# Optimization experiments

Measured on AMD Instinct MI355X. Metric: run time of the kernel, lower is better.

Reference implementation:

```python
import jax, jax.numpy as jnp
import numpy as np

H_LAT = 64   # latent height (original_shape H)
W_LAT = 64   # latent width  (original_shape W)
COND_LEN = 77  # text tokens per regional condition


def _resize_nearest_exact(m, H, W):
    # matches torch F.interpolate(mode='nearest-exact') for a 2D mask
    h0, w0 = m.shape
    ih = jnp.floor((jnp.arange(H) + 0.5) * (h0 / H)).astype(jnp.int32)
    iw = jnp.floor((jnp.arange(W) + 0.5) * (w0 / W)).astype(jnp.int32)
    return m[ih][:, iw]


def setup_inputs() -> dict:
    key = jax.random.key(0)
    kq, kk, kv, km = jax.random.split(key, 4)
    b, qlen, inner = 2, H_LAT * W_LAT, 512
    klen = 4 * COND_LEN  # 4 regions x 77 tokens
    q = jax.random.normal(kq, (b, qlen, inner), dtype=jnp.float32)
    k = jax.random.normal(kk, (b, klen, inner), dtype=jnp.float32)
    v = jax.random.normal(kv, (b, klen, inner), dtype=jnp.float32)
    dd_masks = jax.random.uniform(km, (4, 32, 32), dtype=jnp.float32)
    # ensure full spatial coverage (region 0 = global) so no softmax row is all-masked
    dd_masks = dd_masks.at[0].set(1.0)
    return {"q": q, "k": k, "v": v, "dd_masks": dd_masks, "heads": 8}


def reference(q, k, v, dd_masks, heads):
    b, qlen, inner = q.shape
    dh = inner // heads
    # [b, heads, seq, dh]
    qh = q.reshape(b, qlen, heads, dh).transpose(0, 2, 1, 3)
    kh = k.reshape(b, -1, heads, dh).transpose(0, 2, 1, 3)
    vh = v.reshape(b, -1, heads, dh).transpose(0, 2, 1, 3)

    # build DenseDiffusion mask: each region mask resized to HxW, flattened,
    # and repeated over that region's COND_LEN key columns
    R = dd_masks.shape[0]
    resized = jax.vmap(lambda m: _resize_nearest_exact(m, H_LAT, W_LAT))(dd_masks)  # [R,H,W]
    flat = resized.reshape(R, H_LAT * W_LAT).T            # [HW, R]
    masks = jnp.repeat(flat, COND_LEN, axis=1)            # [HW, R*COND_LEN]
    mask_bool = masks > 0.5                               # [HW, klen]
    mask_scale = (H_LAT * W_LAT) / jnp.sum(masks, axis=0, keepdims=True)  # [1, klen]

    scale = 1.0 / np.sqrt(dh).astype(np.float32)
    attn = jnp.einsum('bhqd,bhkd->bhqk', qh, kh) * scale  # [b,h,HW,klen]
    attn = attn * mask_scale                              # broadcast over b,h,q
    attn = jnp.where(mask_bool, attn, -jnp.inf)
    w = jax.nn.softmax(attn, axis=-1)
    out = jnp.einsum('bhqk,bhkd->bhqd', w, vh)
    return out.transpose(0, 2, 1, 3).reshape(b, qlen, heads * dh)
```

## Files before the change

kernel.cpp:

```cpp
#include <hip/hip_runtime.h>
#include <hip/hip_bf16.h>

typedef __attribute__((ext_vector_type(8))) short short8;
typedef __attribute__((ext_vector_type(4))) float floatx4;

#define HW_TOK 4096
#define KLEN 308
#define DH 64
#define INNER 512

#define VBASE (KLEN * 64)
#define LDS_TOTAL (VBASE + DH * 320)

__device__ __forceinline__ unsigned short f2bf(float f) {
    union { float f; unsigned u; } x; x.f = f;
    unsigned u = x.u;
    return (unsigned short)((u + 0x7FFFu + ((u >> 16) & 1u)) >> 16);
}
__device__ __forceinline__ unsigned pk2bf(float a, float b) {
    return ((unsigned)f2bf(b) << 16) | (unsigned)f2bf(a);
}

__global__ __launch_bounds__(512, 2)
void dd_attn_kernel(const float* __restrict__ q,
                    const float* __restrict__ k,
                    const float* __restrict__ v,
                    const float* __restrict__ dd,
                    float* __restrict__ out) {
    __shared__ unsigned short KV[LDS_TOTAL];

    const int tid  = threadIdx.x;
    const int lane = tid & 63;
    const int wave = tid >> 6;
    const int quad = lane >> 4;
    const int l15  = lane & 15;
    const int kxor = l15 & 7;

    const int bid = blockIdx.x;
    const int bh  = bid >> 5;
    const int grp = bid & 31;
    const int b = bh >> 3, h = bh & 7;

    const float* qp = q + (size_t)b * HW_TOK * INNER + h * DH;
    const float* kp = k + (size_t)b * KLEN * INNER + h * DH;
    const float* vp = v + (size_t)b * KLEN * INNER + h * DH;
    float* op = out + (size_t)b * HW_TOK * INNER + h * DH;

    for (int e = tid; e < KLEN * 32; e += 512) {
        int row = e >> 5, d2 = e & 31;
        float2 f = *(const float2*)(kp + (size_t)row * INNER + 2 * d2);
        int c = d2 >> 2;
        int off = row * 64 + (((c ^ (row & 7)) << 3) | ((d2 & 3) << 1));
        *(unsigned*)&KV[off] = pk2bf(f.x, f.y);
    }
    for (int e = tid; e < KLEN * 32; e += 512) {
        int col = e >> 5, d2 = e & 31;
        float2 f = *(const float2*)(vp + (size_t)col * INNER + 2 * d2);
        int c = col >> 3, c7 = col & 7;
        int r0 = 2 * d2, r1 = r0 + 1;
        KV[VBASE + r0 * 320 + (((c & ~7) | ((c ^ r0) & 7)) << 3) + c7] = f2bf(f.x);
        KV[VBASE + r1 * 320 + (((c & ~7) | ((c ^ r1) & 7)) << 3) + c7] = f2bf(f.y);
    }
    for (int e = tid; e < DH * 12; e += 512) {
        int row = e / 12, col = 308 + e % 12;
        int c = col >> 3, c7 = col & 7;
        KV[VBASE + row * 320 + (((c & ~7) | ((c ^ row) & 7)) << 3) + c7] = 0;
    }

    float rsum = 0.f;
    {
        const float* dp = dd + quad * 1024 + l15 * 4;
        #pragma unroll
        for (int j = 0; j < 16; ++j) {
            float4 f = *(const float4*)(dp + j * 64);
            rsum += f.x + f.y + f.z + f.w;
        }
        #pragma unroll
        for (int off = 1; off < 16; off <<= 1) rsum += __shfl_xor(rsum, off);
    }
    float rsc[4];
    #pragma unroll
    for (int r = 0; r < 4; ++r)
        rsc[r] = 4096.0f / (4.0f * __shfl(rsum, r * 16 + l15));

    __syncthreads();

    const int q0 = (grp * 8 + wave) * 16;
    const int qrow = q0 + l15;

    const float* qr = qp + (size_t)qrow * INNER + quad * 8;
    float4 f0 = *(const float4*)(qr);
    float4 f1 = *(const float4*)(qr + 4);
    float4 f2 = *(const float4*)(qr + 32);
    float4 f3 = *(const float4*)(qr + 36);
    short8 qa0, qa1;
    qa0[0]=(short)f2bf(f0.x); qa0[1]=(short)f2bf(f0.y); qa0[2]=(short)f2bf(f0.z); qa0[3]=(short)f2bf(f0.w);
    qa0[4]=(short)f2bf(f1.x); qa0[5]=(short)f2bf(f1.y); qa0[6]=(short)f2bf(f1.z); qa0[7]=(short)f2bf(f1.w);
    qa1[0]=(short)f2bf(f2.x); qa1[1]=(short)f2bf(f2.y); qa1[2]=(short)f2bf(f2.z); qa1[3]=(short)f2bf(f2.w);
    qa1[4]=(short)f2bf(f3.x); qa1[5]=(short)f2bf(f3.y); qa1[6]=(short)f2bf(f3.z); qa1[7]=(short)f2bf(f3.w);

    const int mi = (qrow >> 7) * 32 + ((qrow & 63) >> 1);
    float coef[4];
    #pragma unroll
    for (int r = 0; r < 4; ++r)
        coef[r] = (dd[r * 1024 + mi] > 0.5f) ? 0.125f * rsc[r] : -1.0f;

    float m_run = -INFINITY, l_run = 0.f;
    floatx4 oacc[4] = {{0,0,0,0},{0,0,0,0},{0,0,0,0},{0,0,0,0}};

    #pragma unroll
    for (int ch = 0; ch < 2; ++ch) {
        floatx4 acc[10];
        #pragma unroll
        for (int t = 0; t < 10; ++t) {
            int row = (ch * 10 + t) * 16 + l15;
            short8 ka0 = *(const short8*)&KV[row * 64 + ((quad       ^ kxor) << 3)];
            short8 ka1 = *(const short8*)&KV[row * 64 + (((4 + quad) ^ kxor) << 3)];
            floatx4 c = {0.f, 0.f, 0.f, 0.f};
            c = __builtin_amdgcn_mfma_f32_16x16x32_bf16(ka0, qa0, c, 0, 0, 0);
            c = __builtin_amdgcn_mfma_f32_16x16x32_bf16(ka1, qa1, c, 0, 0, 0);
            acc[t] = c;
        }

        float mloc = -INFINITY;
        #pragma unroll
        for (int t = 0; t < 10; ++t) {
            #pragma unroll
            for (int r = 0; r < 4; ++r) {
                int kc = (ch * 10 + t) * 16 + quad * 4 + r;
                float cf = (kc < 77) ? coef[0] : (kc < 154) ? coef[1]
                         : (kc < 231) ? coef[2] : (kc < 308) ? coef[3] : -1.0f;
                float sv = (cf > 0.f) ? acc[t][r] * cf : -INFINITY;
                acc[t][r] = sv;
                mloc = fmaxf(mloc, sv);
            }
        }
        mloc = fmaxf(mloc, __shfl_xor(mloc, 16));
        mloc = fmaxf(mloc, __shfl_xor(mloc, 32));

        float m_new = fmaxf(m_run, mloc);
        float alpha = __expf(m_run - m_new);
        float lloc = 0.f;
        #pragma unroll
        for (int t = 0; t < 10; ++t) {
            #pragma unroll
            for (int r = 0; r < 4; ++r) {
                float p = __expf(acc[t][r] - m_new);
                acc[t][r] = p;
                lloc += p;
            }
        }
        lloc += __shfl_xor(lloc, 16);
        lloc += __shfl_xor(lloc, 32);
        l_run = l_run * alpha + lloc;
        m_run = m_new;
        #pragma unroll
        for (int n = 0; n < 4; ++n)
            #pragma unroll
            for (int r = 0; r < 4; ++r) oacc[n][r] *= alpha;

        const int sl0 = ((quad & 1) << 5) + l15;
        const int sl1 = sl0 + 16;
        const bool hi = (quad >= 2);
        #pragma unroll
        for (int c32 = 0; c32 < 5; ++c32) {
            floatx4 pA = acc[2 * c32];
            floatx4 pB = acc[2 * c32 + 1];
            unsigned uA0 = pk2bf(pA[0], pA[1]), uA1 = pk2bf(pA[2], pA[3]);
            unsigned uB0 = pk2bf(pB[0], pB[1]), uB1 = pk2bf(pB[2], pB[3]);
            unsigned xA0 = (unsigned)__shfl((int)uA0, sl0), xB0 = (unsigned)__shfl((int)uB0, sl0);
            unsigned xA1 = (unsigned)__shfl((int)uA1, sl0), xB1 = (unsigned)__shfl((int)uB1, sl0);
            unsigned yA0 = (unsigned)__shfl((int)uA0, sl1), yB0 = (unsigned)__shfl((int)uB0, sl1);
            unsigned yA1 = (unsigned)__shfl((int)uA1, sl1), yB1 = (unsigned)__shfl((int)uB1, sl1);
            union { short8 s; unsigned u[4]; } pu;
            pu.u[0] = hi ? xB0 : xA0;
            pu.u[1] = hi ? xB1 : xA1;
            pu.u[2] = hi ? yB0 : yA0;
            pu.u[3] = hi ? yB1 : yA1;
            #pragma unroll
            for (int n = 0; n < 4; ++n) {
                int row = n * 16 + l15;
                int c = ch * 20 + c32 * 4 + quad;
                int cs = (c & ~7) | ((c ^ kxor) & 7);
                short8 va = *(const short8*)&KV[VBASE + row * 320 + (cs << 3)];
                oacc[n] = __builtin_amdgcn_mfma_f32_16x16x32_bf16(va, pu.s, oacc[n], 0, 0, 0);
            }
        }
    }

    const float inv = 1.0f / l_run;
    #pragma unroll
    for (int n = 0; n < 4; ++n) {
        float4 o;
        o.x = oacc[n][0] * inv;
        o.y = oacc[n][1] * inv;
        o.z = oacc[n][2] * inv;
        o.w = oacc[n][3] * inv;
        *(float4*)&op[(size_t)qrow * INNER + n * 16 + quad * 4] = o;
    }
}

extern "C" void kernel_launch(void* const* d_in, const int* in_sizes, int n_in,
                              void* d_out, int out_size, void* d_ws, size_t ws_size,
                              hipStream_t stream) {
    const float* q  = (const float*)d_in[0];
    const float* k  = (const float*)d_in[1];
    const float* v  = (const float*)d_in[2];
    const float* dd = (const float*)d_in[3];
    float* out = (float*)d_out;
    dd_attn_kernel<<<dim3(512), dim3(512), 0, stream>>>(q, k, v, dd, out);
}
```

Baseline: 105.1 us.

## Process two query tiles per wave to reuse K/V fragments, halve grid

Each wave now handles 32 query rows as two 16-row tiles. Every K and V fragment read from LDS feeds MFMAs for both tiles, and the grid shrinks to 256 blocks, so K/V staging into LDS is repeated half as often. The probability tile now reaches the PV MFMA operand layout through a per-wave LDS buffer instead of cross-lane shuffles. The V transpose staging is rewritten as coalesced per-lane column loads with 16-byte LDS stores. The trade-off is higher register pressure (launch bounds drop to one block per CU) and fewer blocks to hide latency.

```diff
diff --git a/kernel.cpp b/kernel.cpp
--- a/kernel.cpp
+++ b/kernel.cpp
@@ -9,8 +9,11 @@
 #define DH 64
 #define INNER 512
 
-#define VBASE (KLEN * 64)
-#define LDS_TOTAL (VBASE + DH * 320)
+#define KROWS 320
+#define VSTRU 328
+#define VBASE (KROWS * 64)
+#define KV_TOTAL (VBASE + DH * VSTRU)
+#define PSTR 40
 
 __device__ __forceinline__ unsigned short f2bf(float f) {
     union { float f; unsigned u; } x; x.f = f;
@@ -21,24 +24,24 @@
     return ((unsigned)f2bf(b) << 16) | (unsigned)f2bf(a);
 }
 
-__global__ __launch_bounds__(512, 2)
+__global__ __launch_bounds__(512, 1)
 void dd_attn_kernel(const float* __restrict__ q,
                     const float* __restrict__ k,
                     const float* __restrict__ v,
                     const float* __restrict__ dd,
                     float* __restrict__ out) {
-    __shared__ unsigned short KV[LDS_TOTAL];
+    __shared__ unsigned short KV[KV_TOTAL];
+    __shared__ unsigned short Pb[8][2][16][PSTR];
 
     const int tid  = threadIdx.x;
     const int lane = tid & 63;
     const int wave = tid >> 6;
     const int quad = lane >> 4;
     const int l15  = lane & 15;
-    const int kxor = l15 & 7;
 
     const int bid = blockIdx.x;
-    const int bh  = bid >> 5;
-    const int grp = bid & 31;
+    const int bh  = bid >> 4;
+    const int grp = bid & 15;
     const int b = bh >> 3, h = bh & 7;
 
     const float* qp = q + (size_t)b * HW_TOK * INNER + h * DH;
@@ -53,20 +56,21 @@
         int off = row * 64 + (((c ^ (row & 7)) << 3) | ((d2 & 3) << 1));
         *(unsigned*)&KV[off] = pk2bf(f.x, f.y);
     }
-    for (int e = tid; e < KLEN * 32; e += 512) {
-        int col = e >> 5, d2 = e & 31;
-        float2 f = *(const float2*)(vp + (size_t)col * INNER + 2 * d2);
-        int c = col >> 3, c7 = col & 7;
-        int r0 = 2 * d2, r1 = r0 + 1;
-        KV[VBASE + r0 * 320 + (((c & ~7) | ((c ^ r0) & 7)) << 3) + c7] = f2bf(f.x);
-        KV[VBASE + r1 * 320 + (((c & ~7) | ((c ^ r1) & 7)) << 3) + c7] = f2bf(f.y);
-    }
-    for (int e = tid; e < DH * 12; e += 512) {
-        int row = e / 12, col = 308 + e % 12;
-        int c = col >> 3, c7 = col & 7;
-        KV[VBASE + row * 320 + (((c & ~7) | ((c ^ row) & 7)) << 3) + c7] = 0;
-    }
-
+    #pragma unroll
+    for (int i = 0; i < 5; ++i) {
+        int cq = wave + 8 * i;
+        float f[8];
+        #pragma unroll
+        for (int j = 0; j < 8; ++j) {
+            int col = cq * 8 + j;
+            f[j] = (col < KLEN) ? vp[(size_t)col * INNER + lane] : 0.f;
+        }
+        union { short8 s; unsigned u[4]; } vv;
+        #pragma unroll
+        for (int j = 0; j < 4; ++j) vv.u[j] = pk2bf(f[2 * j], f[2 * j + 1]);
+        int swz = (cq & ~7) | ((cq ^ (lane & 7)) & 7);
+        *(short8*)&KV[VBASE + lane * VSTRU + (swz << 3)] = vv.s;
+    }
     float rsum = 0.f;
     {
         const float* dp = dd + quad * 1024 + l15 * 4;
@@ -85,118 +89,138 @@
 
     __syncthreads();
 
-    const int q0 = (grp * 8 + wave) * 16;
-    const int qrow = q0 + l15;
-
-    const float* qr = qp + (size_t)qrow * INNER + quad * 8;
-    float4 f0 = *(const float4*)(qr);
-    float4 f1 = *(const float4*)(qr + 4);
-    float4 f2 = *(const float4*)(qr + 32);
-    float4 f3 = *(const float4*)(qr + 36);
-    short8 qa0, qa1;
-    qa0[0]=(short)f2bf(f0.x); qa0[1]=(short)f2bf(f0.y); qa0[2]=(short)f2bf(f0.z); qa0[3]=(short)f2bf(f0.w);
-    qa0[4]=(short)f2bf(f1.x); qa0[5]=(short)f2bf(f1.y); qa0[6]=(short)f2bf(f1.z); qa0[7]=(short)f2bf(f1.w);
-    qa1[0]=(short)f2bf(f2.x); qa1[1]=(short)f2bf(f2.y); qa1[2]=(short)f2bf(f2.z); qa1[3]=(short)f2bf(f2.w);
-    qa1[4]=(short)f2bf(f3.x); qa1[5]=(short)f2bf(f3.y); qa1[6]=(short)f2bf(f3.z); qa1[7]=(short)f2bf(f3.w);
-
-    const int mi = (qrow >> 7) * 32 + ((qrow & 63) >> 1);
-    float coef[4];
-    #pragma unroll
-    for (int r = 0; r < 4; ++r)
-        coef[r] = (dd[r * 1024 + mi] > 0.5f) ? 0.125f * rsc[r] : -1.0f;
-
-    float m_run = -INFINITY, l_run = 0.f;
-    floatx4 oacc[4] = {{0,0,0,0},{0,0,0,0},{0,0,0,0},{0,0,0,0}};
-
-    #pragma unroll
-    for (int ch = 0; ch < 2; ++ch) {
-        floatx4 acc[10];
-        #pragma unroll
-        for (int t = 0; t < 10; ++t) {
-            int row = (ch * 10 + t) * 16 + l15;
-            short8 ka0 = *(const short8*)&KV[row * 64 + ((quad       ^ kxor) << 3)];
-            short8 ka1 = *(const short8*)&KV[row * 64 + (((4 + quad) ^ kxor) << 3)];
-            floatx4 c = {0.f, 0.f, 0.f, 0.f};
-            c = __builtin_amdgcn_mfma_f32_16x16x32_bf16(ka0, qa0, c, 0, 0, 0);
-            c = __builtin_amdgcn_mfma_f32_16x16x32_bf16(ka1, qa1, c, 0, 0, 0);
-            acc[t] = c;
-        }
-
-        float mloc = -INFINITY;
-        #pragma unroll
-        for (int t = 0; t < 10; ++t) {
-            #pragma unroll
-            for (int r = 0; r < 4; ++r) {
-                int kc = (ch * 10 + t) * 16 + quad * 4 + r;
-                float cf = (kc < 77) ? coef[0] : (kc < 154) ? coef[1]
-                         : (kc < 231) ? coef[2] : (kc < 308) ? coef[3] : -1.0f;
-                float sv = (cf > 0.f) ? acc[t][r] * cf : -INFINITY;
-                acc[t][r] = sv;
-                mloc = fmaxf(mloc, sv);
-            }
-        }
-        mloc = fmaxf(mloc, __shfl_xor(mloc, 16));
-        mloc = fmaxf(mloc, __shfl_xor(mloc, 32));
-
-        float m_new = fmaxf(m_run, mloc);
-        float alpha = __expf(m_run - m_new);
-        float lloc = 0.f;
-        #pragma unroll
-        for (int t = 0; t < 10; ++t) {
-            #pragma unroll
-            for (int r = 0; r < 4; ++r) {
-                float p = __expf(acc[t][r] - m_new);
-                acc[t][r] = p;
-                lloc += p;
-            }
-        }
-        lloc += __shfl_xor(lloc, 16);
-        lloc += __shfl_xor(lloc, 32);
-        l_run = l_run * alpha + lloc;
-        m_run = m_new;
-        #pragma unroll
-        for (int n = 0; n < 4; ++n)
-            #pragma unroll
-            for (int r = 0; r < 4; ++r) oacc[n][r] *= alpha;
-
-        const int sl0 = ((quad & 1) << 5) + l15;
-        const int sl1 = sl0 + 16;
-        const bool hi = (quad >= 2);
-        #pragma unroll
-        for (int c32 = 0; c32 < 5; ++c32) {
-            floatx4 pA = acc[2 * c32];
-            floatx4 pB = acc[2 * c32 + 1];
-            unsigned uA0 = pk2bf(pA[0], pA[1]), uA1 = pk2bf(pA[2], pA[3]);
-            unsigned uB0 = pk2bf(pB[0], pB[1]), uB1 = pk2bf(pB[2], pB[3]);
-            unsigned xA0 = (unsigned)__shfl((int)uA0, sl0), xB0 = (unsigned)__shfl((int)uB0, sl0);
-            unsigned xA1 = (unsigned)__shfl((int)uA1, sl0), xB1 = (unsigned)__shfl((int)uB1, sl0);
-            unsigned yA0 = (unsigned)__shfl((int)uA0, sl1), yB0 = (unsigned)__shfl((int)uB0, sl1);
-            unsigned yA1 = (unsigned)__shfl((int)uA1, sl1), yB1 = (unsigned)__shfl((int)uB1, sl1);
-            union { short8 s; unsigned u[4]; } pu;
-            pu.u[0] = hi ? xB0 : xA0;
-            pu.u[1] = hi ? xB1 : xA1;
-            pu.u[2] = hi ? yB0 : yA0;
-            pu.u[3] = hi ? yB1 : yA1;
+    const int q0 = (grp * 8 + wave) * 32;
+
+    short8 qa[2][2];
+    #pragma unroll
+    for (int qt = 0; qt < 2; ++qt) {
+        const float* qr = qp + (size_t)(q0 + qt * 16 + l15) * INNER + quad * 8;
+        float4 g0 = *(const float4*)(qr);
+        float4 g1 = *(const float4*)(qr + 4);
+        float4 g2 = *(const float4*)(qr + 32);
+        float4 g3 = *(const float4*)(qr + 36);
+        union { short8 s; unsigned u[4]; } ua, ub;
+        ua.u[0] = pk2bf(g0.x, g0.y); ua.u[1] = pk2bf(g0.z, g0.w);
+        ua.u[2] = pk2bf(g1.x, g1.y); ua.u[3] = pk2bf(g1.z, g1.w);
+        ub.u[0] = pk2bf(g2.x, g2.y); ub.u[1] = pk2bf(g2.z, g2.w);
+        ub.u[2] = pk2bf(g3.x, g3.y); ub.u[3] = pk2bf(g3.z, g3.w);
+        qa[qt][0] = ua.s; qa[qt][1] = ub.s;
+    }
+    float coef[2][4];
+    #pragma unroll
+    for (int qt = 0; qt < 2; ++qt) {
+        int qrow = q0 + qt * 16 + l15;
+        int mi = (qrow >> 7) * 32 + ((qrow & 63) >> 1);
+        #pragma unroll
+        for (int r = 0; r < 4; ++r)
+            coef[qt][r] = (dd[r * 1024 + mi] > 0.5f) ? 0.125f * rsc[r] : -1.0f;
+    }
+
+    float m_run[2] = {-INFINITY, -INFINITY};
+    float l_run[2] = {0.f, 0.f};
+    floatx4 oacc[2][4] = {{{0,0,0,0},{0,0,0,0},{0,0,0,0},{0,0,0,0}},
+                          {{0,0,0,0},{0,0,0,0},{0,0,0,0},{0,0,0,0}}};
+
+    #pragma unroll
+    for (int ch = 0; ch < 4; ++ch) {
+        const int NT = (ch < 3) ? 6 : 2;
+        floatx4 acc[2][6];
+
+        #pragma unroll
+        for (int t = 0; t < NT; ++t) {
+            int row = (ch * 6 + t) * 16 + l15;
+            short8 ka0 = *(const short8*)&KV[row * 64 + (((quad    ) ^ (row & 7)) << 3)];
+            short8 ka1 = *(const short8*)&KV[row * 64 + (((4 + quad) ^ (row & 7)) << 3)];
+            #pragma unroll
+            for (int qt = 0; qt < 2; ++qt) {
+                floatx4 c = {0.f, 0.f, 0.f, 0.f};
+                c = __builtin_amdgcn_mfma_f32_16x16x32_bf16(ka0, qa[qt][0], c, 0, 0, 0);
+                c = __builtin_amdgcn_mfma_f32_16x16x32_bf16(ka1, qa[qt][1], c, 0, 0, 0);
+                acc[qt][t] = c;
+            }
+        }
+
+        #pragma unroll
+        for (int qt = 0; qt < 2; ++qt) {
+            float mloc = -INFINITY;
+            #pragma unroll
+            for (int t = 0; t < NT; ++t) {
+                #pragma unroll
+                for (int r = 0; r < 4; ++r) {
+                    int kc = (ch * 6 + t) * 16 + quad * 4 + r;
+                    float cf = (kc < 77) ? coef[qt][0] : (kc < 154) ? coef[qt][1]
+                             : (kc < 231) ? coef[qt][2] : (kc < 308) ? coef[qt][3] : -1.0f;
+                    float sv = (cf > 0.f) ? acc[qt][t][r] * cf : -INFINITY;
+                    acc[qt][t][r] = sv;
+                    mloc = fmaxf(mloc, sv);
+                }
+            }
+            mloc = fmaxf(mloc, __shfl_xor(mloc, 16));
+            mloc = fmaxf(mloc, __shfl_xor(mloc, 32));
+            float m_new = fmaxf(m_run[qt], mloc);
+            float alpha = __expf(m_run[qt] - m_new);
+            float lloc = 0.f;
+            #pragma unroll
+            for (int t = 0; t < NT; ++t) {
+                #pragma unroll
+                for (int r = 0; r < 4; ++r) {
+                    float p = __expf(acc[qt][t][r] - m_new);
+                    acc[qt][t][r] = p;
+                    lloc += p;
+                }
+            }
+            lloc += __shfl_xor(lloc, 16);
+            lloc += __shfl_xor(lloc, 32);
+            l_run[qt] = l_run[qt] * alpha + lloc;
+            m_run[qt] = m_new;
+            #pragma unroll
+            for (int n = 0; n < 4; ++n)
+                #pragma unroll
+                for (int r = 0; r < 4; ++r) oacc[qt][n][r] *= alpha;
+        }
+
+        const int NS = NT / 2;
+        #pragma unroll
+        for (int s = 0; s < NS; ++s) {
+            #pragma unroll
+            for (int qt = 0; qt < 2; ++qt) {
+                unsigned p0 = pk2bf(acc[qt][2*s][0],     acc[qt][2*s][1]);
+                unsigned p1 = pk2bf(acc[qt][2*s][2],     acc[qt][2*s][3]);
+                unsigned p2 = pk2bf(acc[qt][2*s+1][0],   acc[qt][2*s+1][1]);
+                unsigned p3 = pk2bf(acc[qt][2*s+1][2],   acc[qt][2*s+1][3]);
+                *(uint2*)&Pb[wave][qt][l15][quad * 4]      = make_uint2(p0, p1);
+                *(uint2*)&Pb[wave][qt][l15][16 + quad * 4] = make_uint2(p2, p3);
+            }
+            short8 pbv[2];
+            #pragma unroll
+            for (int qt = 0; qt < 2; ++qt)
+                pbv[qt] = *(const short8*)&Pb[wave][qt][l15][quad * 8];
             #pragma unroll
             for (int n = 0; n < 4; ++n) {
                 int row = n * 16 + l15;
-                int c = ch * 20 + c32 * 4 + quad;
-                int cs = (c & ~7) | ((c ^ kxor) & 7);
-                short8 va = *(const short8*)&KV[VBASE + row * 320 + (cs << 3)];
-                oacc[n] = __builtin_amdgcn_mfma_f32_16x16x32_bf16(va, pu.s, oacc[n], 0, 0, 0);
-            }
-        }
-    }
-
-    const float inv = 1.0f / l_run;
-    #pragma unroll
-    for (int n = 0; n < 4; ++n) {
-        float4 o;
-        o.x = oacc[n][0] * inv;
-        o.y = oacc[n][1] * inv;
-        o.z = oacc[n][2] * inv;
-        o.w = oacc[n][3] * inv;
-        *(float4*)&op[(size_t)qrow * INNER + n * 16 + quad * 4] = o;
+                int cq = ch * 12 + s * 4 + quad;
+                int swz = (cq & ~7) | ((cq ^ (row & 7)) & 7);
+                short8 va = *(const short8*)&KV[VBASE + row * VSTRU + (swz << 3)];
+                #pragma unroll
+                for (int qt = 0; qt < 2; ++qt)
+                    oacc[qt][n] = __builtin_amdgcn_mfma_f32_16x16x32_bf16(va, pbv[qt], oacc[qt][n], 0, 0, 0);
+            }
+        }
+    }
+
+    #pragma unroll
+    for (int qt = 0; qt < 2; ++qt) {
+        float inv = 1.0f / l_run[qt];
+        float* o = op + (size_t)(q0 + qt * 16 + l15) * INNER + quad * 4;
+        #pragma unroll
+        for (int n = 0; n < 4; ++n) {
+            float4 ov;
+            ov.x = oacc[qt][n][0] * inv;
+            ov.y = oacc[qt][n][1] * inv;
+            ov.z = oacc[qt][n][2] * inv;
+            ov.w = oacc[qt][n][3] * inv;
+            *(float4*)&o[n * 16] = ov;
+        }
     }
 }
 
@@ -208,5 +232,5 @@
     const float* v  = (const float*)d_in[2];
     const float* dd = (const float*)d_in[3];
     float* out = (float*)d_out;
-    dd_attn_kernel<<<dim3(512), dim3(512), 0, stream>>>(q, k, v, dd, out);
-}
+    dd_attn_kernel<<<dim3(256), dim3(512), 0, stream>>>(q, k, v, dd, out);
+}
```

New measurement: 93.59 us. -11.0%, faster.
